# Kernel tuning notes

Hardware: AMD Instinct MI355X
Metric: run time of the kernel (lower is better)

The kernel has to match this reference:

```python
import jax, jax.numpy as jnp
import numpy as np

N0, N1, N2, F, H, O, B = 1_000_000, 200_000, 40_000, 128, 64, 64, 1024
EPS = 1e-5


def _bn(h, g, b):
    # BatchNorm1d, training mode: biased batch statistics over the node dim
    m = h.mean(0)
    v = jnp.mean(jnp.square(h - m), 0)
    return (h - m) * jax.lax.rsqrt(v + EPS) * g + b


def _mlp(h, Wa, ba, ga, bea, Wb, bb, gb, beb):
    h = jax.nn.relu(_bn(h @ Wa + ba, ga, bea))
    h = jax.nn.relu(_bn(h @ Wb + bb, gb, beb))
    return h


def _conv(x, src, dst, n_out, params):
    # scatter-add aggregation: out[dst] += x[src]  (flow=target_to_source, aggr=add)
    agg = jax.ops.segment_sum(x[src], dst, num_segments=n_out)
    return _mlp(agg, *params)


def setup_inputs() -> dict:
    key = jax.random.key(0)
    ks = jax.random.split(key, 12)

    def lin(k, i, o):
        return (jax.random.normal(k, (i, o), jnp.float32) / np.sqrt(i)).astype(jnp.float32)

    d = {}
    d["x"] = jax.random.normal(ks[0], (N0, F), jnp.float32)
    d["e1_dst"] = jax.random.randint(ks[1], (N0,), 0, N1, jnp.int32)
    d["e1_src"] = jnp.arange(N0, dtype=jnp.int32)
    d["e2_dst"] = jax.random.randint(ks[2], (N1,), 0, N2, jnp.int32)
    d["e2_src"] = jnp.arange(N1, dtype=jnp.int32)
    d["batch1"] = jnp.sort(jax.random.randint(ks[3], (N1,), 0, B, jnp.int32))
    d["batch2"] = jnp.sort(jax.random.randint(ks[4], (N2,), 0, B, jnp.int32))
    # conv1 MLP params
    d["W1a"] = lin(ks[5], F, H); d["b1a"] = jnp.zeros((H,), jnp.float32)
    d["g1a"] = jnp.ones((H,), jnp.float32); d["be1a"] = jnp.zeros((H,), jnp.float32)
    d["W1b"] = lin(ks[6], H, H); d["b1b"] = jnp.zeros((H,), jnp.float32)
    d["g1b"] = jnp.ones((H,), jnp.float32); d["be1b"] = jnp.zeros((H,), jnp.float32)
    # conv2 MLP params
    d["W2a"] = lin(ks[7], H, H); d["b2a"] = jnp.zeros((H,), jnp.float32)
    d["g2a"] = jnp.ones((H,), jnp.float32); d["be2a"] = jnp.zeros((H,), jnp.float32)
    d["W2b"] = lin(ks[8], H, H); d["b2b"] = jnp.zeros((H,), jnp.float32)
    d["g2b"] = jnp.ones((H,), jnp.float32); d["be2b"] = jnp.zeros((H,), jnp.float32)
    # dim_align: Linear(nhid*num_convs, output_dim), dropout p=0 -> identity
    d["Wout"] = lin(ks[9], 2 * H, O); d["bout"] = jnp.zeros((O,), jnp.float32)
    d["num_graphs"] = B
    return d


def reference(x, e1_dst, e1_src, e2_dst, e2_src, batch1, batch2,
              W1a, b1a, g1a, be1a, W1b, b1b, g1b, be1b,
              W2a, b2a, g2a, be2a, W2b, b2b, g2b, be2b,
              Wout, bout, num_graphs):
    n1 = batch1.shape[0]
    n2 = batch2.shape[0]
    x1 = _conv(x, e1_src, e1_dst, n1, (W1a, b1a, g1a, be1a, W1b, b1b, g1b, be1b))
    x2 = _conv(x1, e2_src, e2_dst, n2, (W2a, b2a, g2a, be2a, W2b, b2b, g2b, be2b))
    # global sum pooling per layer, then concat and dim_align
    p1 = jax.ops.segment_sum(x1, batch1, num_segments=num_graphs)
    p2 = jax.ops.segment_sum(x2, batch2, num_segments=num_graphs)
    pooled = jnp.concatenate([p1, p2], axis=1)  # [B, 2H]
    return pooled @ Wout + bout
```

## Files before the change

kernel.cpp:

```cpp
#include <hip/hip_runtime.h>

#define N0 1000000
#define N1 200000
#define N2 40000
#define FDIM 128
#define HDIM 64
#define ODIM 64
#define NB 1024
#define EPSV 1e-5f
#define NCHUNK 196
#define GCHUNK 64
#define NGW 15625
#define NREP 32

__global__ __launch_bounds__(256) void k_hist(const int* __restrict__ dst,
                                              int* __restrict__ deg)
{
  int i = blockIdx.x * 256 + threadIdx.x;
  const int stride = gridDim.x * 256;
  for (; i < N0; i += stride) atomicAdd(&deg[dst[i]], 1);
}

__global__ __launch_bounds__(256) void k_scanA(const int* __restrict__ deg,
                                               int* __restrict__ csum)
{
  __shared__ int red[256];
  const int b = blockIdx.x, t = threadIdx.x;
  const int base = b * 1024 + t * 4;
  int s = 0;
#pragma unroll
  for (int j = 0; j < 4; ++j) {
    int i = base + j;
    if (i < N1) s += deg[i];
  }
  red[t] = s;
  __syncthreads();
  for (int off = 128; off > 0; off >>= 1) {
    if (t < off) red[t] += red[t + off];
    __syncthreads();
  }
  if (t == 0) csum[b] = red[0];
}

__global__ __launch_bounds__(256) void k_scanC(const int* __restrict__ deg,
                                               const int* __restrict__ csum,
                                               int* __restrict__ off,
                                               int* __restrict__ cur)
{
  __shared__ int red[256];
  __shared__ int top[256];
  const int b = blockIdx.x, t = threadIdx.x;
  top[t] = (t < NCHUNK) ? csum[t] : 0;
  const int base = b * 1024 + t * 4;
  int v[4];
  int s = 0;
#pragma unroll
  for (int j = 0; j < 4; ++j) {
    int i = base + j;
    v[j] = (i < N1) ? deg[i] : 0;
    s += v[j];
  }
  red[t] = s;
  __syncthreads();
  for (int o = 1; o < 256; o <<= 1) {
    int addR = (t >= o) ? red[t - o] : 0;
    int addT = (t >= o) ? top[t - o] : 0;
    __syncthreads();
    red[t] += addR;
    top[t] += addT;
    __syncthreads();
  }
  const int cbase = (b == 0) ? 0 : top[b - 1];
  int start = cbase + red[t] - s;
#pragma unroll
  for (int j = 0; j < 4; ++j) {
    int i = base + j;
    if (i < N1) { off[i] = start; cur[i] = start; }
    start += v[j];
  }
  if (b == NCHUNK - 1 && t == 255) off[N1] = start;
}

__global__ __launch_bounds__(256) void k_fill(const int* __restrict__ dst,
                                              int* __restrict__ cur,
                                              int* __restrict__ eidx)
{
  int i = blockIdx.x * 256 + threadIdx.x;
  const int stride = gridDim.x * 256;
  for (; i < N0; i += stride) {
    int p = atomicAdd(&cur[dst[i]], 1);
    eidx[p] = i;
  }
}

__device__ __forceinline__ int lowerb(const int* __restrict__ a, int n, int v)
{
  int lo = 0, hi = n;
  while (lo < hi) {
    int mid = (lo + hi) >> 1;
    if (a[mid] < v) lo = mid + 1; else hi = mid;
  }
  return lo;
}

__global__ __launch_bounds__(256) void k_wstart(const int* __restrict__ off,
                                                int* __restrict__ ws)
{
  int w = blockIdx.x * 256 + threadIdx.x;
  if (w < NGW) ws[w] = lowerb(off, N1 + 1, w * GCHUNK);
}

__global__ __launch_bounds__(128) void k_conv1(
    const float* __restrict__ x, const int* __restrict__ off,
    const int* __restrict__ ws, const int* __restrict__ eidx,
    const float* __restrict__ W, float* __restrict__ out,
    float* __restrict__ stats)
{
  __shared__ float xs[FDIM];
  __shared__ float ps[2][2][HDIM];
  const int lane = threadIdx.x & 63;
  const int hf = threadIdx.x >> 6;
  const int wid = blockIdx.x;
  const int d0 = ws[wid];
  const int d1 = (wid == NGW - 1) ? N1 : ws[wid + 1];
  if (d0 >= d1) return;
  float w[HDIM];
#pragma unroll
  for (int k = 0; k < HDIM; ++k) w[k] = W[(hf * HDIM + k) * HDIM + lane];
  const float* xh = x + hf * HDIM + lane;
  const int e_start = off[d0];
  const int e_end = off[d1];
  int d = d0;
  int nend = off[d0 + 1];
  int parity = 0;
  float acc = 0.f;
  float ss = 0.f, qq = 0.f;

  auto FLUSH = [&]() {
    xs[hf * HDIM + lane] = acc;
    float p = 0.f;
#pragma unroll
    for (int kk = 0; kk < HDIM; ++kk) p = fmaf(xs[hf * HDIM + kk], w[kk], p);
    ps[parity][hf][lane] = p;
    __syncthreads();
    if (hf == 0) {
      float h = ps[parity][0][lane] + ps[parity][1][lane];
      out[(size_t)d * HDIM + lane] = h;
      ss += h;
      qq += h * h;
    }
    parity ^= 1;
    acc = 0.f;
    ++d;
    nend = off[min(d + 1, N1)];
  };

  int j = e_start;
  while (j < e_end) {
    const int cnt = min(64, e_end - j);
    int myidx = eidx[min(j + lane, N0 - 1)];
    int k = 0;
    for (; k + 8 <= cnt; k += 8) {
      int id[8];
#pragma unroll
      for (int u = 0; u < 8; ++u) id[u] = __shfl(myidx, k + u);
      float v[8];
#pragma unroll
      for (int u = 0; u < 8; ++u) v[u] = xh[(size_t)id[u] * FDIM];
#pragma unroll
      for (int u = 0; u < 8; ++u) {
        while (j + k + u == nend) FLUSH();
        acc += v[u];
      }
    }
    for (; k < cnt; ++k) {
      int id0 = __shfl(myidx, k);
      float v0 = xh[(size_t)id0 * FDIM];
      while (j + k == nend) FLUSH();
      acc += v0;
    }
    j += cnt;
  }
  while (d < d1) FLUSH();

  if (hf == 0) {
    float* rep = stats + (size_t)(wid & (NREP - 1)) * 2 * HDIM;
    unsafeAtomicAdd(&rep[lane], ss);
    unsafeAtomicAdd(&rep[HDIM + lane], qq);
  }
}

template <bool BNIN, bool STATS>
__global__ __launch_bounds__(256) void k_gemm64(
    const float* __restrict__ in, int M, const float* __restrict__ W,
    const float* __restrict__ sumsIn, int nrep, const float* __restrict__ g,
    const float* __restrict__ be, float invN,
    float* __restrict__ out, float* __restrict__ osum, float* __restrict__ osq)
{
  __shared__ __align__(16) float xs[4][HDIM * 4];
  __shared__ float AC[2][HDIM];
  const int lane = threadIdx.x & 63;
  const int wv = threadIdx.x >> 6;
  if constexpr (BNIN) {
    if (threadIdx.x < 64) {
      float sm = 0.f, sq = 0.f;
      for (int r = 0; r < nrep; ++r) {
        sm += sumsIn[r * 2 * HDIM + threadIdx.x];
        sq += sumsIn[r * 2 * HDIM + HDIM + threadIdx.x];
      }
      float m = sm * invN;
      float var = sq * invN - m * m;
      float a = rsqrtf(var + EPSV) * g[threadIdx.x];
      AC[0][threadIdx.x] = a;
      AC[1][threadIdx.x] = be[threadIdx.x] - m * a;
    }
    __syncthreads();
  }
  float w[HDIM];
#pragma unroll
  for (int k = 0; k < HDIM; ++k) w[k] = W[k * HDIM + lane];
  const int r = lane >> 4;
  const int seg = lane & 15;
  float4 av = make_float4(1.f, 1.f, 1.f, 1.f);
  float4 cv = make_float4(0.f, 0.f, 0.f, 0.f);
  if constexpr (BNIN) {
    av = *(const float4*)&AC[0][seg * 4];
    cv = *(const float4*)&AC[1][seg * 4];
  }
  float ss = 0.f, qq = 0.f;
  const int sweep = gridDim.x * 16;
  for (int base = (blockIdx.x * 4 + wv) * 4; base < M; base += sweep) {
    float4 v = *(const float4*)(in + (size_t)(base + r) * HDIM + seg * 4);
    if constexpr (BNIN) {
      v.x = fmaxf(0.f, fmaf(v.x, av.x, cv.x));
      v.y = fmaxf(0.f, fmaf(v.y, av.y, cv.y));
      v.z = fmaxf(0.f, fmaf(v.z, av.z, cv.z));
      v.w = fmaxf(0.f, fmaf(v.w, av.w, cv.w));
    }
    const int k0 = seg * 4;
    xs[wv][(k0 + 0) * 4 + r] = v.x;
    xs[wv][(k0 + 1) * 4 + r] = v.y;
    xs[wv][(k0 + 2) * 4 + r] = v.z;
    xs[wv][(k0 + 3) * 4 + r] = v.w;
    float a0 = 0.f, a1 = 0.f, a2 = 0.f, a3 = 0.f;
#pragma unroll
    for (int k = 0; k < HDIM; ++k) {
      float4 xv = *(const float4*)&xs[wv][k * 4];
      a0 = fmaf(xv.x, w[k], a0);
      a1 = fmaf(xv.y, w[k], a1);
      a2 = fmaf(xv.z, w[k], a2);
      a3 = fmaf(xv.w, w[k], a3);
    }
    out[(size_t)(base + 0) * HDIM + lane] = a0;
    out[(size_t)(base + 1) * HDIM + lane] = a1;
    out[(size_t)(base + 2) * HDIM + lane] = a2;
    out[(size_t)(base + 3) * HDIM + lane] = a3;
    if constexpr (STATS) {
      ss += a0 + a1 + a2 + a3;
      qq += a0 * a0 + a1 * a1 + a2 * a2 + a3 * a3;
    }
  }
  if constexpr (STATS) {
    __shared__ float red[2][4][HDIM];
    red[0][wv][lane] = ss;
    red[1][wv][lane] = qq;
    __syncthreads();
    if (wv == 0) {
      float s = red[0][0][lane] + red[0][1][lane] + red[0][2][lane] + red[0][3][lane];
      float q = red[1][0][lane] + red[1][1][lane] + red[1][2][lane] + red[1][3][lane];
      unsafeAtomicAdd(&osum[lane], s);
      unsafeAtomicAdd(&osq[lane], q);
    }
  }
}

template <bool SCATTER>
__global__ __launch_bounds__(256) void k_bnrelu_pool(
    const float* __restrict__ in, const float* __restrict__ sumsIn,
    const float* __restrict__ g, const float* __restrict__ be, float invN,
    const int* __restrict__ dst, float* __restrict__ agg,
    const int* __restrict__ batch, float* __restrict__ pool, int M)
{
  const int lane = threadIdx.x & 63;
  const int wv = threadIdx.x >> 6;
  const int nw = gridDim.x * 4;
  const int wid = blockIdx.x * 4 + wv;
  const int chunk = (M + nw - 1) / nw;
  int r0 = wid * chunk;
  int r1 = min(M, r0 + chunk);
  if (r0 >= r1) return;
  const float m = sumsIn[lane] * invN;
  const float var = sumsIn[64 + lane] * invN - m * m;
  const float a = rsqrtf(var + EPSV) * g[lane];
  const float c = be[lane] - m * a;
  int curb = batch[r0];
  float pacc = 0.f;
  for (int row = r0; row < r1; ++row) {
    float v = fmaxf(0.f, fmaf(in[(size_t)row * HDIM + lane], a, c));
    if constexpr (SCATTER)
      unsafeAtomicAdd(&agg[(size_t)dst[row] * HDIM + lane], v);
    int b = batch[row];
    if (b != curb) {
      unsafeAtomicAdd(&pool[(size_t)curb * HDIM + lane], pacc);
      pacc = 0.f;
      curb = b;
    }
    pacc += v;
  }
  unsafeAtomicAdd(&pool[(size_t)curb * HDIM + lane], pacc);
}

__global__ __launch_bounds__(256) void k_final(
    const float* __restrict__ p1, const float* __restrict__ p2,
    const float* __restrict__ Wout, const float* __restrict__ bo,
    float* __restrict__ out)
{
  const int row = blockIdx.x * 4 + (threadIdx.x >> 6);
  const int j = threadIdx.x & 63;
  const float* q1 = p1 + (size_t)row * HDIM;
  const float* q2 = p2 + (size_t)row * HDIM;
  float acc = bo[j];
#pragma unroll
  for (int k = 0; k < HDIM; ++k) acc = fmaf(q1[k], Wout[k * ODIM + j], acc);
#pragma unroll
  for (int k = 0; k < HDIM; ++k) acc = fmaf(q2[k], Wout[(HDIM + k) * ODIM + j], acc);
  out[(size_t)row * ODIM + j] = acc;
}

extern "C" void kernel_launch(void* const* d_in, const int* in_sizes, int n_in,
                              void* d_out, int out_size, void* d_ws, size_t ws_size,
                              hipStream_t stream)
{
  (void)in_sizes; (void)n_in; (void)out_size; (void)ws_size;
  const float* x      = (const float*)d_in[0];
  const int*  e1_dst  = (const int*)d_in[1];
  const int*  e2_dst  = (const int*)d_in[3];
  const int*  batch1  = (const int*)d_in[5];
  const int*  batch2  = (const int*)d_in[6];
  const float* W1a  = (const float*)d_in[7];
  const float* g1a  = (const float*)d_in[9];
  const float* be1a = (const float*)d_in[10];
  const float* W1b  = (const float*)d_in[11];
  const float* g1b  = (const float*)d_in[13];
  const float* be1b = (const float*)d_in[14];
  const float* W2a  = (const float*)d_in[15];
  const float* g2a  = (const float*)d_in[17];
  const float* be2a = (const float*)d_in[18];
  const float* W2b  = (const float*)d_in[19];
  const float* g2b  = (const float*)d_in[21];
  const float* be2b = (const float*)d_in[22];
  const float* Wout = (const float*)d_in[23];
  const float* bout = (const float*)d_in[24];

  float* ws = (float*)d_ws;
  float* h1pre = ws;
  float* h2pre = h1pre + (size_t)N1 * HDIM;
  float* agg2  = h2pre + (size_t)N1 * HDIM;
  float* h3pre = agg2 + (size_t)N2 * HDIM;
  float* h4pre = h3pre + (size_t)N2 * HDIM;
  float* p1    = h4pre + (size_t)N2 * HDIM;
  float* p2    = p1 + (size_t)NB * HDIM;
  float* st1   = p2 + (size_t)NB * HDIM;
  float* st2   = st1 + NREP * 2 * HDIM;
  float* st3   = st2 + 2 * HDIM;
  float* st4   = st3 + 2 * HDIM;
  int* deg  = (int*)(st4 + 2 * HDIM);
  int* off  = deg + N1;
  int* cur  = off + N1 + 1;
  int* csum = cur + N1;
  int* eidx = csum + ((NCHUNK + 63) & ~63);
  int* wsa  = eidx + N0;

  hipMemsetAsync(deg, 0, (size_t)N1 * sizeof(int), stream);
  hipMemsetAsync(agg2, 0, (size_t)N2 * HDIM * sizeof(float), stream);
  hipMemsetAsync(p1, 0,
                 (2 * (size_t)NB * HDIM + (NREP + 3) * 2 * HDIM) * sizeof(float),
                 stream);

  k_hist<<<1024, 256, 0, stream>>>(e1_dst, deg);
  k_scanA<<<NCHUNK, 256, 0, stream>>>(deg, csum);
  k_scanC<<<NCHUNK, 256, 0, stream>>>(deg, csum, off, cur);
  k_fill<<<1024, 256, 0, stream>>>(e1_dst, cur, eidx);
  k_wstart<<<(NGW + 255) / 256, 256, 0, stream>>>(off, wsa);

  k_conv1<<<NGW, 128, 0, stream>>>(x, off, wsa, eidx, W1a, h1pre, st1);
  k_gemm64<true, true><<<1024, 256, 0, stream>>>(
      h1pre, N1, W1b, st1, NREP, g1a, be1a, 1.f / N1, h2pre,
      st2, st2 + HDIM);
  k_bnrelu_pool<true><<<1024, 256, 0, stream>>>(
      h2pre, st2, g1b, be1b, 1.f / N1, e2_dst, agg2, batch1, p1, N1);
  k_gemm64<false, true><<<512, 256, 0, stream>>>(
      agg2, N2, W2a, nullptr, 0, nullptr, nullptr, 0.f, h3pre,
      st3, st3 + HDIM);
  k_gemm64<true, true><<<512, 256, 0, stream>>>(
      h3pre, N2, W2b, st3, 1, g2a, be2a, 1.f / N2, h4pre,
      st4, st4 + HDIM);
  k_bnrelu_pool<false><<<512, 256, 0, stream>>>(
      h4pre, st4, g2b, be2b, 1.f / N2, nullptr, nullptr, batch2, p2, N2);
  k_final<<<NB / 4, 256, 0, stream>>>(p1, p2, Wout, bout, (float*)d_out);
}
```

Baseline: 490.7 us.

## Replace conv2 atomic scatter with CSR gather and vectorize conv1 flush dot

Builds a second CSR (histogram, scan, fill, wave starts) for the layer-2 edges. The per-row float atomic scatter into agg2 is replaced by a dedicated gather kernel that applies BN+ReLU on the fly and writes each destination row once, so the agg2 memset is no longer needed. The conv1 flush dot product now uses float4 LDS reads with four independent accumulators. It adds five small setup kernels and a second read of h2pre, in exchange for removing contended atomics.

```diff
diff --git a/kernel.cpp b/kernel.cpp
--- a/kernel.cpp
+++ b/kernel.cpp
@@ -8,21 +8,23 @@
 #define ODIM 64
 #define NB 1024
 #define EPSV 1e-5f
-#define NCHUNK 196
 #define GCHUNK 64
-#define NGW 15625
+#define NGW1 15625
+#define NGW2 3125
+#define NCHUNK1 196
+#define NCHUNK2 40
 #define NREP 32
 
 __global__ __launch_bounds__(256) void k_hist(const int* __restrict__ dst,
-                                              int* __restrict__ deg)
+                                              int* __restrict__ deg, int E)
 {
   int i = blockIdx.x * 256 + threadIdx.x;
   const int stride = gridDim.x * 256;
-  for (; i < N0; i += stride) atomicAdd(&deg[dst[i]], 1);
+  for (; i < E; i += stride) atomicAdd(&deg[dst[i]], 1);
 }
 
 __global__ __launch_bounds__(256) void k_scanA(const int* __restrict__ deg,
-                                               int* __restrict__ csum)
+                                               int* __restrict__ csum, int M)
 {
   __shared__ int red[256];
   const int b = blockIdx.x, t = threadIdx.x;
@@ -31,7 +33,7 @@
 #pragma unroll
   for (int j = 0; j < 4; ++j) {
     int i = base + j;
-    if (i < N1) s += deg[i];
+    if (i < M) s += deg[i];
   }
   red[t] = s;
   __syncthreads();
@@ -45,19 +47,20 @@
 __global__ __launch_bounds__(256) void k_scanC(const int* __restrict__ deg,
                                                const int* __restrict__ csum,
                                                int* __restrict__ off,
-                                               int* __restrict__ cur)
+                                               int* __restrict__ cur,
+                                               int M, int nchunk)
 {
   __shared__ int red[256];
   __shared__ int top[256];
   const int b = blockIdx.x, t = threadIdx.x;
-  top[t] = (t < NCHUNK) ? csum[t] : 0;
+  top[t] = (t < nchunk) ? csum[t] : 0;
   const int base = b * 1024 + t * 4;
   int v[4];
   int s = 0;
 #pragma unroll
   for (int j = 0; j < 4; ++j) {
     int i = base + j;
-    v[j] = (i < N1) ? deg[i] : 0;
+    v[j] = (i < M) ? deg[i] : 0;
     s += v[j];
   }
   red[t] = s;
@@ -75,19 +78,19 @@
 #pragma unroll
   for (int j = 0; j < 4; ++j) {
     int i = base + j;
-    if (i < N1) { off[i] = start; cur[i] = start; }
+    if (i < M) { off[i] = start; cur[i] = start; }
     start += v[j];
   }
-  if (b == NCHUNK - 1 && t == 255) off[N1] = start;
+  if (b == nchunk - 1 && t == 255) off[M] = start;
 }
 
 __global__ __launch_bounds__(256) void k_fill(const int* __restrict__ dst,
                                               int* __restrict__ cur,
-                                              int* __restrict__ eidx)
+                                              int* __restrict__ eidx, int E)
 {
   int i = blockIdx.x * 256 + threadIdx.x;
   const int stride = gridDim.x * 256;
-  for (; i < N0; i += stride) {
+  for (; i < E; i += stride) {
     int p = atomicAdd(&cur[dst[i]], 1);
     eidx[p] = i;
   }
@@ -104,10 +107,11 @@
 }
 
 __global__ __launch_bounds__(256) void k_wstart(const int* __restrict__ off,
-                                                int* __restrict__ ws)
+                                                int* __restrict__ ws,
+                                                int M, int ngw)
 {
   int w = blockIdx.x * 256 + threadIdx.x;
-  if (w < NGW) ws[w] = lowerb(off, N1 + 1, w * GCHUNK);
+  if (w < ngw) ws[w] = lowerb(off, M + 1, w * GCHUNK);
 }
 
 __global__ __launch_bounds__(128) void k_conv1(
@@ -116,13 +120,13 @@
     const float* __restrict__ W, float* __restrict__ out,
     float* __restrict__ stats)
 {
-  __shared__ float xs[FDIM];
+  __shared__ __align__(16) float xs[FDIM];
   __shared__ float ps[2][2][HDIM];
   const int lane = threadIdx.x & 63;
   const int hf = threadIdx.x >> 6;
   const int wid = blockIdx.x;
   const int d0 = ws[wid];
-  const int d1 = (wid == NGW - 1) ? N1 : ws[wid + 1];
+  const int d1 = (wid == NGW1 - 1) ? N1 : ws[wid + 1];
   if (d0 >= d1) return;
   float w[HDIM];
 #pragma unroll
@@ -138,10 +142,16 @@
 
   auto FLUSH = [&]() {
     xs[hf * HDIM + lane] = acc;
-    float p = 0.f;
-#pragma unroll
-    for (int kk = 0; kk < HDIM; ++kk) p = fmaf(xs[hf * HDIM + kk], w[kk], p);
-    ps[parity][hf][lane] = p;
+    float p0 = 0.f, p1v = 0.f, p2v = 0.f, p3v = 0.f;
+#pragma unroll
+    for (int kk = 0; kk < HDIM; kk += 4) {
+      float4 xv = *(const float4*)&xs[hf * HDIM + kk];
+      p0  = fmaf(xv.x, w[kk + 0], p0);
+      p1v = fmaf(xv.y, w[kk + 1], p1v);
+      p2v = fmaf(xv.z, w[kk + 2], p2v);
+      p3v = fmaf(xv.w, w[kk + 3], p3v);
+    }
+    ps[parity][hf][lane] = (p0 + p1v) + (p2v + p3v);
     __syncthreads();
     if (hf == 0) {
       float h = ps[parity][0][lane] + ps[parity][1][lane];
@@ -188,6 +198,65 @@
     unsafeAtomicAdd(&rep[lane], ss);
     unsafeAtomicAdd(&rep[HDIM + lane], qq);
   }
+}
+
+__global__ __launch_bounds__(256) void k_gather2(
+    const float* __restrict__ h2, const int* __restrict__ off,
+    const int* __restrict__ ws, const int* __restrict__ eidx,
+    const float* __restrict__ sumsIn, const float* __restrict__ g,
+    const float* __restrict__ be, float invN, float* __restrict__ agg)
+{
+  const int wid = blockIdx.x * 4 + (threadIdx.x >> 6);
+  if (wid >= NGW2) return;
+  const int lane = threadIdx.x & 63;
+  const int d0 = ws[wid];
+  const int d1 = (wid == NGW2 - 1) ? N2 : ws[wid + 1];
+  if (d0 >= d1) return;
+  const float m = sumsIn[lane] * invN;
+  const float var = sumsIn[HDIM + lane] * invN - m * m;
+  const float a = rsqrtf(var + EPSV) * g[lane];
+  const float c = be[lane] - m * a;
+  const int e_start = off[d0];
+  const int e_end = off[d1];
+  int d = d0;
+  int nend = off[d0 + 1];
+  float acc = 0.f;
+
+  auto FLUSH = [&]() {
+    agg[(size_t)d * HDIM + lane] = acc;
+    acc = 0.f;
+    ++d;
+    nend = off[min(d + 1, N2)];
+  };
+
+  int j = e_start;
+  while (j < e_end) {
+    const int cnt = min(64, e_end - j);
+    int myidx = eidx[min(j + lane, N1 - 1)];
+    int k = 0;
+    for (; k + 8 <= cnt; k += 8) {
+      int id[8];
+#pragma unroll
+      for (int u = 0; u < 8; ++u) id[u] = __shfl(myidx, k + u);
+      float v[8];
+#pragma unroll
+      for (int u = 0; u < 8; ++u)
+        v[u] = fmaxf(0.f, fmaf(h2[(size_t)id[u] * HDIM + lane], a, c));
+#pragma unroll
+      for (int u = 0; u < 8; ++u) {
+        while (j + k + u == nend) FLUSH();
+        acc += v[u];
+      }
+    }
+    for (; k < cnt; ++k) {
+      int id0 = __shfl(myidx, k);
+      float v0 = fmaxf(0.f, fmaf(h2[(size_t)id0 * HDIM + lane], a, c));
+      while (j + k == nend) FLUSH();
+      acc += v0;
+    }
+    j += cnt;
+  }
+  while (d < d1) FLUSH();
 }
 
 template <bool BNIN, bool STATS>
@@ -274,11 +343,9 @@
   }
 }
 
-template <bool SCATTER>
-__global__ __launch_bounds__(256) void k_bnrelu_pool(
+__global__ __launch_bounds__(256) void k_pool_bn(
     const float* __restrict__ in, const float* __restrict__ sumsIn,
     const float* __restrict__ g, const float* __restrict__ be, float invN,
-    const int* __restrict__ dst, float* __restrict__ agg,
     const int* __restrict__ batch, float* __restrict__ pool, int M)
 {
   const int lane = threadIdx.x & 63;
@@ -297,8 +364,6 @@
   float pacc = 0.f;
   for (int row = r0; row < r1; ++row) {
     float v = fmaxf(0.f, fmaf(in[(size_t)row * HDIM + lane], a, c));
-    if constexpr (SCATTER)
-      unsafeAtomicAdd(&agg[(size_t)dst[row] * HDIM + lane], v);
     int b = batch[row];
     if (b != curb) {
       unsafeAtomicAdd(&pool[(size_t)curb * HDIM + lane], pacc);
@@ -364,38 +429,50 @@
   float* st2   = st1 + NREP * 2 * HDIM;
   float* st3   = st2 + 2 * HDIM;
   float* st4   = st3 + 2 * HDIM;
-  int* deg  = (int*)(st4 + 2 * HDIM);
-  int* off  = deg + N1;
-  int* cur  = off + N1 + 1;
-  int* csum = cur + N1;
-  int* eidx = csum + ((NCHUNK + 63) & ~63);
-  int* wsa  = eidx + N0;
-
-  hipMemsetAsync(deg, 0, (size_t)N1 * sizeof(int), stream);
-  hipMemsetAsync(agg2, 0, (size_t)N2 * HDIM * sizeof(float), stream);
+  int* deg1  = (int*)(st4 + 2 * HDIM);
+  int* deg2  = deg1 + N1;
+  int* off1  = deg2 + N2;
+  int* cur1  = off1 + N1 + 1;
+  int* csum1 = cur1 + N1;
+  int* eidx1 = csum1 + 256;
+  int* ws1   = eidx1 + N0;
+  int* off2  = ws1 + NGW1;
+  int* cur2  = off2 + N2 + 1;
+  int* csum2 = cur2 + N2;
+  int* eidx2 = csum2 + 256;
+  int* ws2   = eidx2 + N1;
+
+  hipMemsetAsync(deg1, 0, (size_t)(N1 + N2) * sizeof(int), stream);
   hipMemsetAsync(p1, 0,
                  (2 * (size_t)NB * HDIM + (NREP + 3) * 2 * HDIM) * sizeof(float),
                  stream);
 
-  k_hist<<<1024, 256, 0, stream>>>(e1_dst, deg);
-  k_scanA<<<NCHUNK, 256, 0, stream>>>(deg, csum);
-  k_scanC<<<NCHUNK, 256, 0, stream>>>(deg, csum, off, cur);
-  k_fill<<<1024, 256, 0, stream>>>(e1_dst, cur, eidx);
-  k_wstart<<<(NGW + 255) / 256, 256, 0, stream>>>(off, wsa);
-
-  k_conv1<<<NGW, 128, 0, stream>>>(x, off, wsa, eidx, W1a, h1pre, st1);
+  k_hist<<<1024, 256, 0, stream>>>(e1_dst, deg1, N0);
+  k_scanA<<<NCHUNK1, 256, 0, stream>>>(deg1, csum1, N1);
+  k_scanC<<<NCHUNK1, 256, 0, stream>>>(deg1, csum1, off1, cur1, N1, NCHUNK1);
+  k_fill<<<1024, 256, 0, stream>>>(e1_dst, cur1, eidx1, N0);
+  k_wstart<<<(NGW1 + 255) / 256, 256, 0, stream>>>(off1, ws1, N1, NGW1);
+  k_hist<<<256, 256, 0, stream>>>(e2_dst, deg2, N1);
+  k_scanA<<<NCHUNK2, 256, 0, stream>>>(deg2, csum2, N2);
+  k_scanC<<<NCHUNK2, 256, 0, stream>>>(deg2, csum2, off2, cur2, N2, NCHUNK2);
+  k_fill<<<256, 256, 0, stream>>>(e2_dst, cur2, eidx2, N1);
+  k_wstart<<<(NGW2 + 255) / 256, 256, 0, stream>>>(off2, ws2, N2, NGW2);
+
+  k_conv1<<<NGW1, 128, 0, stream>>>(x, off1, ws1, eidx1, W1a, h1pre, st1);
   k_gemm64<true, true><<<1024, 256, 0, stream>>>(
       h1pre, N1, W1b, st1, NREP, g1a, be1a, 1.f / N1, h2pre,
       st2, st2 + HDIM);
-  k_bnrelu_pool<true><<<1024, 256, 0, stream>>>(
-      h2pre, st2, g1b, be1b, 1.f / N1, e2_dst, agg2, batch1, p1, N1);
+  k_gather2<<<(NGW2 + 3) / 4, 256, 0, stream>>>(
+      h2pre, off2, ws2, eidx2, st2, g1b, be1b, 1.f / N1, agg2);
+  k_pool_bn<<<1024, 256, 0, stream>>>(
+      h2pre, st2, g1b, be1b, 1.f / N1, batch1, p1, N1);
   k_gemm64<false, true><<<512, 256, 0, stream>>>(
       agg2, N2, W2a, nullptr, 0, nullptr, nullptr, 0.f, h3pre,
       st3, st3 + HDIM);
   k_gemm64<true, true><<<512, 256, 0, stream>>>(
       h3pre, N2, W2b, st3, 1, g2a, be2a, 1.f / N2, h4pre,
       st4, st4 + HDIM);
-  k_bnrelu_pool<false><<<512, 256, 0, stream>>>(
-      h4pre, st4, g2b, be2b, 1.f / N2, nullptr, nullptr, batch2, p2, N2);
+  k_pool_bn<<<512, 256, 0, stream>>>(
+      h4pre, st4, g2b, be2b, 1.f / N2, batch2, p2, N2);
   k_final<<<NB / 4, 256, 0, stream>>>(p1, p2, Wout, bout, (float*)d_out);
 }
```

Result: slower. 500.9 us (+2.1%).

## Split conv1 feature halves into independent wavefronts with atomic output accumulation

Applied to the files above, without the earlier changes.

Each conv1 work chunk is now handled by two separate wavefronts, one per 64-feature half of the input. Each wavefront computes its partial 64x64 projection per destination node and atomically adds it into a pre-zeroed output, so the per-node block barrier is gone. BatchNorm statistics move out of conv1 into a separate k_stats pass over h1pre. This costs an extra memset and an extra read of the 200k x 64 buffer, plus atomic traffic on every output element.

```diff
diff --git a/kernel.cpp b/kernel.cpp
--- a/kernel.cpp
+++ b/kernel.cpp
@@ -8,21 +8,20 @@
 #define ODIM 64
 #define NB 1024
 #define EPSV 1e-5f
-#define NCHUNK 196
 #define GCHUNK 64
-#define NGW 15625
-#define NREP 32
+#define NGW1 15625
+#define NCHUNK1 196
 
 __global__ __launch_bounds__(256) void k_hist(const int* __restrict__ dst,
-                                              int* __restrict__ deg)
+                                              int* __restrict__ deg, int E)
 {
   int i = blockIdx.x * 256 + threadIdx.x;
   const int stride = gridDim.x * 256;
-  for (; i < N0; i += stride) atomicAdd(&deg[dst[i]], 1);
+  for (; i < E; i += stride) atomicAdd(&deg[dst[i]], 1);
 }
 
 __global__ __launch_bounds__(256) void k_scanA(const int* __restrict__ deg,
-                                               int* __restrict__ csum)
+                                               int* __restrict__ csum, int M)
 {
   __shared__ int red[256];
   const int b = blockIdx.x, t = threadIdx.x;
@@ -31,7 +30,7 @@
 #pragma unroll
   for (int j = 0; j < 4; ++j) {
     int i = base + j;
-    if (i < N1) s += deg[i];
+    if (i < M) s += deg[i];
   }
   red[t] = s;
   __syncthreads();
@@ -45,19 +44,20 @@
 __global__ __launch_bounds__(256) void k_scanC(const int* __restrict__ deg,
                                                const int* __restrict__ csum,
                                                int* __restrict__ off,
-                                               int* __restrict__ cur)
+                                               int* __restrict__ cur,
+                                               int M, int nchunk)
 {
   __shared__ int red[256];
   __shared__ int top[256];
   const int b = blockIdx.x, t = threadIdx.x;
-  top[t] = (t < NCHUNK) ? csum[t] : 0;
+  top[t] = (t < nchunk) ? csum[t] : 0;
   const int base = b * 1024 + t * 4;
   int v[4];
   int s = 0;
 #pragma unroll
   for (int j = 0; j < 4; ++j) {
     int i = base + j;
-    v[j] = (i < N1) ? deg[i] : 0;
+    v[j] = (i < M) ? deg[i] : 0;
     s += v[j];
   }
   red[t] = s;
@@ -75,19 +75,19 @@
 #pragma unroll
   for (int j = 0; j < 4; ++j) {
     int i = base + j;
-    if (i < N1) { off[i] = start; cur[i] = start; }
+    if (i < M) { off[i] = start; cur[i] = start; }
     start += v[j];
   }
-  if (b == NCHUNK - 1 && t == 255) off[N1] = start;
+  if (b == nchunk - 1 && t == 255) off[M] = start;
 }
 
 __global__ __launch_bounds__(256) void k_fill(const int* __restrict__ dst,
                                               int* __restrict__ cur,
-                                              int* __restrict__ eidx)
+                                              int* __restrict__ eidx, int E)
 {
   int i = blockIdx.x * 256 + threadIdx.x;
   const int stride = gridDim.x * 256;
-  for (; i < N0; i += stride) {
+  for (; i < E; i += stride) {
     int p = atomicAdd(&cur[dst[i]], 1);
     eidx[p] = i;
   }
@@ -104,25 +104,27 @@
 }
 
 __global__ __launch_bounds__(256) void k_wstart(const int* __restrict__ off,
-                                                int* __restrict__ ws)
+                                                int* __restrict__ ws,
+                                                int M, int ngw)
 {
   int w = blockIdx.x * 256 + threadIdx.x;
-  if (w < NGW) ws[w] = lowerb(off, N1 + 1, w * GCHUNK);
-}
-
-__global__ __launch_bounds__(128) void k_conv1(
+  if (w < ngw) ws[w] = lowerb(off, M + 1, w * GCHUNK);
+}
+
+__global__ __launch_bounds__(256) void k_conv1(
     const float* __restrict__ x, const int* __restrict__ off,
     const int* __restrict__ ws, const int* __restrict__ eidx,
-    const float* __restrict__ W, float* __restrict__ out,
-    float* __restrict__ stats)
-{
-  __shared__ float xs[FDIM];
-  __shared__ float ps[2][2][HDIM];
+    const float* __restrict__ W, float* __restrict__ out)
+{
+  __shared__ __align__(16) float xs[4][HDIM];
   const int lane = threadIdx.x & 63;
-  const int hf = threadIdx.x >> 6;
-  const int wid = blockIdx.x;
+  const int wv = threadIdx.x >> 6;
+  const int gw = blockIdx.x * 4 + wv;
+  if (gw >= 2 * NGW1) return;
+  const int wid = gw >> 1;
+  const int hf = gw & 1;
   const int d0 = ws[wid];
-  const int d1 = (wid == NGW - 1) ? N1 : ws[wid + 1];
+  const int d1 = (wid == NGW1 - 1) ? N1 : ws[wid + 1];
   if (d0 >= d1) return;
   float w[HDIM];
 #pragma unroll
@@ -132,24 +134,20 @@
   const int e_end = off[d1];
   int d = d0;
   int nend = off[d0 + 1];
-  int parity = 0;
   float acc = 0.f;
-  float ss = 0.f, qq = 0.f;
 
   auto FLUSH = [&]() {
-    xs[hf * HDIM + lane] = acc;
-    float p = 0.f;
-#pragma unroll
-    for (int kk = 0; kk < HDIM; ++kk) p = fmaf(xs[hf * HDIM + kk], w[kk], p);
-    ps[parity][hf][lane] = p;
-    __syncthreads();
-    if (hf == 0) {
-      float h = ps[parity][0][lane] + ps[parity][1][lane];
-      out[(size_t)d * HDIM + lane] = h;
-      ss += h;
-      qq += h * h;
-    }
-    parity ^= 1;
+    xs[wv][lane] = acc;
+    float p0 = 0.f, p1 = 0.f, p2 = 0.f, p3 = 0.f;
+#pragma unroll
+    for (int kk = 0; kk < HDIM; kk += 4) {
+      float4 xv = *(const float4*)&xs[wv][kk];
+      p0 = fmaf(xv.x, w[kk + 0], p0);
+      p1 = fmaf(xv.y, w[kk + 1], p1);
+      p2 = fmaf(xv.z, w[kk + 2], p2);
+      p3 = fmaf(xv.w, w[kk + 3], p3);
+    }
+    unsafeAtomicAdd(&out[(size_t)d * HDIM + lane], (p0 + p1) + (p2 + p3));
     acc = 0.f;
     ++d;
     nend = off[min(d + 1, N1)];
@@ -182,18 +180,36 @@
     j += cnt;
   }
   while (d < d1) FLUSH();
-
-  if (hf == 0) {
-    float* rep = stats + (size_t)(wid & (NREP - 1)) * 2 * HDIM;
-    unsafeAtomicAdd(&rep[lane], ss);
-    unsafeAtomicAdd(&rep[HDIM + lane], qq);
+}
+
+__global__ __launch_bounds__(256) void k_stats(
+    const float* __restrict__ in, int M,
+    float* __restrict__ osum, float* __restrict__ osq)
+{
+  const int col = threadIdx.x & 63;
+  const int rw = threadIdx.x >> 6;
+  float s = 0.f, q = 0.f;
+  for (int row = blockIdx.x * 4 + rw; row < M; row += gridDim.x * 4) {
+    float v = in[(size_t)row * HDIM + col];
+    s += v;
+    q += v * v;
+  }
+  __shared__ float red[2][4][HDIM];
+  red[0][rw][col] = s;
+  red[1][rw][col] = q;
+  __syncthreads();
+  if (rw == 0) {
+    s = red[0][0][col] + red[0][1][col] + red[0][2][col] + red[0][3][col];
+    q = red[1][0][col] + red[1][1][col] + red[1][2][col] + red[1][3][col];
+    unsafeAtomicAdd(&osum[col], s);
+    unsafeAtomicAdd(&osq[col], q);
   }
 }
 
 template <bool BNIN, bool STATS>
 __global__ __launch_bounds__(256) void k_gemm64(
     const float* __restrict__ in, int M, const float* __restrict__ W,
-    const float* __restrict__ sumsIn, int nrep, const float* __restrict__ g,
+    const float* __restrict__ sumsIn, const float* __restrict__ g,
     const float* __restrict__ be, float invN,
     float* __restrict__ out, float* __restrict__ osum, float* __restrict__ osq)
 {
@@ -203,13 +219,8 @@
   const int wv = threadIdx.x >> 6;
   if constexpr (BNIN) {
     if (threadIdx.x < 64) {
-      float sm = 0.f, sq = 0.f;
-      for (int r = 0; r < nrep; ++r) {
-        sm += sumsIn[r * 2 * HDIM + threadIdx.x];
-        sq += sumsIn[r * 2 * HDIM + HDIM + threadIdx.x];
-      }
-      float m = sm * invN;
-      float var = sq * invN - m * m;
+      float m = sumsIn[threadIdx.x] * invN;
+      float var = sumsIn[64 + threadIdx.x] * invN - m * m;
       float a = rsqrtf(var + EPSV) * g[threadIdx.x];
       AC[0][threadIdx.x] = a;
       AC[1][threadIdx.x] = be[threadIdx.x] - m * a;
@@ -361,40 +372,39 @@
   float* p1    = h4pre + (size_t)N2 * HDIM;
   float* p2    = p1 + (size_t)NB * HDIM;
   float* st1   = p2 + (size_t)NB * HDIM;
-  float* st2   = st1 + NREP * 2 * HDIM;
+  float* st2   = st1 + 2 * HDIM;
   float* st3   = st2 + 2 * HDIM;
   float* st4   = st3 + 2 * HDIM;
-  int* deg  = (int*)(st4 + 2 * HDIM);
-  int* off  = deg + N1;
-  int* cur  = off + N1 + 1;
-  int* csum = cur + N1;
-  int* eidx = csum + ((NCHUNK + 63) & ~63);
-  int* wsa  = eidx + N0;
-
-  hipMemsetAsync(deg, 0, (size_t)N1 * sizeof(int), stream);
+  int* deg1  = (int*)(st4 + 2 * HDIM);
+  int* off1  = deg1 + N1;
+  int* cur1  = off1 + N1 + 1;
+  int* csum1 = cur1 + N1;
+  int* eidx1 = csum1 + 256;
+  int* ws1   = eidx1 + N0;
+
+  hipMemsetAsync(deg1, 0, (size_t)N1 * sizeof(int), stream);
+  hipMemsetAsync(h1pre, 0, (size_t)N1 * HDIM * sizeof(float), stream);
   hipMemsetAsync(agg2, 0, (size_t)N2 * HDIM * sizeof(float), stream);
-  hipMemsetAsync(p1, 0,
-                 (2 * (size_t)NB * HDIM + (NREP + 3) * 2 * HDIM) * sizeof(float),
+  hipMemsetAsync(p1, 0, (2 * (size_t)NB * HDIM + 4 * 2 * HDIM) * sizeof(float),
                  stream);
 
-  k_hist<<<1024, 256, 0, stream>>>(e1_dst, deg);
-  k_scanA<<<NCHUNK, 256, 0, stream>>>(deg, csum);
-  k_scanC<<<NCHUNK, 256, 0, stream>>>(deg, csum, off, cur);
-  k_fill<<<1024, 256, 0, stream>>>(e1_dst, cur, eidx);
-  k_wstart<<<(NGW + 255) / 256, 256, 0, stream>>>(off, wsa);
-
-  k_conv1<<<NGW, 128, 0, stream>>>(x, off, wsa, eidx, W1a, h1pre, st1);
+  k_hist<<<1024, 256, 0, stream>>>(e1_dst, deg1, N0);
+  k_scanA<<<NCHUNK1, 256, 0, stream>>>(deg1, csum1, N1);
+  k_scanC<<<NCHUNK1, 256, 0, stream>>>(deg1, csum1, off1, cur1, N1, NCHUNK1);
+  k_fill<<<1024, 256, 0, stream>>>(e1_dst, cur1, eidx1, N0);
+  k_wstart<<<(NGW1 + 255) / 256, 256, 0, stream>>>(off1, ws1, N1, NGW1);
+
+  k_conv1<<<(2 * NGW1 + 3) / 4, 256, 0, stream>>>(x, off1, ws1, eidx1, W1a,
+                                                  h1pre);
+  k_stats<<<1024, 256, 0, stream>>>(h1pre, N1, st1, st1 + HDIM);
   k_gemm64<true, true><<<1024, 256, 0, stream>>>(
-      h1pre, N1, W1b, st1, NREP, g1a, be1a, 1.f / N1, h2pre,
-      st2, st2 + HDIM);
+      h1pre, N1, W1b, st1, g1a, be1a, 1.f / N1, h2pre, st2, st2 + HDIM);
   k_bnrelu_pool<true><<<1024, 256, 0, stream>>>(
       h2pre, st2, g1b, be1b, 1.f / N1, e2_dst, agg2, batch1, p1, N1);
   k_gemm64<false, true><<<512, 256, 0, stream>>>(
-      agg2, N2, W2a, nullptr, 0, nullptr, nullptr, 0.f, h3pre,
-      st3, st3 + HDIM);
+      agg2, N2, W2a, nullptr, nullptr, nullptr, 0.f, h3pre, st3, st3 + HDIM);
   k_gemm64<true, true><<<512, 256, 0, stream>>>(
-      h3pre, N2, W2b, st3, 1, g2a, be2a, 1.f / N2, h4pre,
-      st4, st4 + HDIM);
+      h3pre, N2, W2b, st3, g2a, be2a, 1.f / N2, h4pre, st4, st4 + HDIM);
   k_bnrelu_pool<false><<<512, 256, 0, stream>>>(
       h4pre, st4, g2b, be2b, 1.f / N2, nullptr, nullptr, batch2, p2, N2);
   k_final<<<NB / 4, 256, 0, stream>>>(p1, p2, Wout, bout, (float*)d_out);
```

Result: slower. 576.1 us (+17.4%).
